# Kernel optimization log

Hardware: AMD Instinct MI355X
Metric: run time of the kernel (lower is better)

Reference implementation:

```python
import jax, jax.numpy as jnp
import numpy as np

HIDDEN = 1024
INTER = 2048
NUM_EXPERTS = 8
TOP_K = 2
GROUP_SIZE = 128
TOKENS = 4096


def _dequant_int4(packed, scale, group_size):
    # packed: [E, N, K//2] ints in [0,256) holding two uint4 nibbles (low | high<<4)
    # scale:  [E, N, K//group_size] float32
    E, N, Kh = packed.shape
    K = 2 * Kh
    low = packed & 0xF
    high = (packed >> 4) & 0xF
    # interleave: even K positions = low nibble, odd = high nibble
    q = jnp.stack([low, high], axis=-1).reshape(E, N, K) - 8  # int4 values in [-8,7]
    q = q.astype(jnp.float32).reshape(E, N, K // group_size, group_size)
    w = q * scale[..., None]
    return w.reshape(E, N, K)


def setup_inputs() -> dict:
    key = jax.random.key(0)
    k1, k2, k3, k4, k5, k6 = jax.random.split(key, 6)
    x = jax.random.normal(k1, (TOKENS, HIDDEN), dtype=jnp.float32)
    router_w = jax.random.normal(k2, (NUM_EXPERTS, HIDDEN), dtype=jnp.float32) * 0.02
    w1 = jax.random.randint(k3, (NUM_EXPERTS, 2 * INTER, HIDDEN // 2), 0, 256, dtype=jnp.int32)
    w1_scale = jax.random.uniform(k4, (NUM_EXPERTS, 2 * INTER, HIDDEN // GROUP_SIZE), dtype=jnp.float32) * 0.05
    w2 = jax.random.randint(k5, (NUM_EXPERTS, HIDDEN, INTER // 2), 0, 256, dtype=jnp.int32)
    w2_scale = jax.random.uniform(k6, (NUM_EXPERTS, HIDDEN, INTER // GROUP_SIZE), dtype=jnp.float32) * 0.05
    return {"x": x, "router_w": router_w, "w1": w1, "w1_scale": w1_scale, "w2": w2, "w2_scale": w2_scale}


def reference(x, router_w, w1, w1_scale, w2, w2_scale):
    # Router: topk then softmax over the top-k logits
    scores = x @ router_w.T                                 # [T, E]
    top_w, top_i = jax.lax.top_k(scores, TOP_K)             # [T, K]
    top_w = jax.nn.softmax(top_w, axis=-1).astype(jnp.float32)

    # Dequantize int4 grouped weights once
    w1_deq = _dequant_int4(w1, w1_scale, GROUP_SIZE)        # [E, 2I, H]
    w2_deq = _dequant_int4(w2, w2_scale, GROUP_SIZE)        # [E, H, I]

    out = jnp.zeros_like(x)
    for e in range(NUM_EXPERTS):
        # per-token routing weight for expert e (0 if not routed)
        ge = jnp.sum(top_w * (top_i == e), axis=-1)         # [T]
        h = x @ w1_deq[e].T                                  # [T, 2I]
        gate, up = h[:, :INTER], h[:, INTER:]
        a = jax.nn.silu(gate) * up                           # SwiGLU
        y = a @ w2_deq[e].T                                  # [T, H]
        out = out + ge[:, None] * y
    return out
```

## Files before the change

### kernel.cpp

```cpp
#include <hip/hip_runtime.h>
#include <hip/hip_bf16.h>

#define HIDDEN 1024
#define INTER 2048
#define NE 8
#define GS 128
#define TOKENS 4096
#define MAXROWS 9216
#define MAXTILES 72

typedef __bf16 bf16x8 __attribute__((ext_vector_type(8)));
typedef float f32x4 __attribute__((ext_vector_type(4)));

#define OFF_TOPKI 0u
#define OFF_TOPKW 32768u
#define OFF_CTRL  65536u
#define OFF_TOK   66048u
#define OFF_SLOT  102912u
#define OFF_TILE  135680u
#define OFF_XB    139776u
#define OFF_A     8530432u
#define OFF_W1D   46279168u
#define OFF_W2D   113388032u
#define OFF_Y0    OFF_W1D
#define OFF_Y1    (OFF_W1D + 18874368u)

__device__ __forceinline__ unsigned short f2bf(float f) {
  union { float f; unsigned int u; } v; v.f = f;
  unsigned int r = (v.u + 0x7FFFu + ((v.u >> 16) & 1u)) >> 16;
  return (unsigned short)r;
}
__device__ __forceinline__ float bf2f(unsigned int u) {
  union { unsigned int u; float f; } v; v.u = u << 16;
  return v.f;
}
__device__ __forceinline__ unsigned int pack2(unsigned short lo, unsigned short hi) {
  return (unsigned int)lo | ((unsigned int)hi << 16);
}

typedef const __attribute__((address_space(1))) unsigned int GAS;
typedef __attribute__((address_space(3))) unsigned int LAS;
__device__ __forceinline__ void gload16(const unsigned short* g, unsigned short* l) {
  __builtin_amdgcn_global_load_lds((GAS*)g, (LAS*)l, 16, 0, 0);
}


__global__ __launch_bounds__(256) void k_prep(const float* __restrict__ x,
    const float* __restrict__ rw, int* __restrict__ topki, float* __restrict__ topkw,
    const int* __restrict__ w1, const float* __restrict__ w1s,
    unsigned short* __restrict__ w1d,
    const int* __restrict__ w2, const float* __restrict__ w2s,
    unsigned short* __restrict__ w2d, unsigned short* __restrict__ xb) {
  int bid = blockIdx.x, tid = threadIdx.x;
  if (bid == 25600) {
    uint2 z; z.x = 0u; z.y = 0u;
    *reinterpret_cast<uint2*>(xb + (size_t)TOKENS * HIDDEN + tid * 4) = z;
    return;
  }
  if (bid >= 17408) {
    int gid = (bid - 17408) * 256 + tid;
    int i4 = gid * 4;
    int r = i4 >> 10;
    int i = i4 & 1023;
    float s = w2s[r * 16 + (i >> 6)];
    int4 p = *reinterpret_cast<const int4*>(w2 + (size_t)i4);
    int pv[4] = { p.x, p.y, p.z, p.w };
    uint4 o; unsigned int ov[4];
#pragma unroll
    for (int j = 0; j < 4; j++) {
      float lo = (float)((pv[j] & 15) - 8) * s;
      float hi = (float)(((pv[j] >> 4) & 15) - 8) * s;
      ov[j] = pack2(f2bf(lo), f2bf(hi));
    }
    o.x = ov[0]; o.y = ov[1]; o.z = ov[2]; o.w = ov[3];
    *reinterpret_cast<uint4*>(w2d + ((size_t)r << 11) + 2 * i) = o;
    return;
  }
  if (bid >= 1024) {
    int gid = (bid - 1024) * 256 + tid;
    int i4 = gid * 4;
    int r = i4 >> 9;
    int i = i4 & 511;
    float s = w1s[r * 8 + (i >> 6)];
    int4 p = *reinterpret_cast<const int4*>(w1 + (size_t)i4);
    int pv[4] = { p.x, p.y, p.z, p.w };
    uint4 o; unsigned int ov[4];
#pragma unroll
    for (int j = 0; j < 4; j++) {
      float lo = (float)((pv[j] & 15) - 8) * s;
      float hi = (float)(((pv[j] >> 4) & 15) - 8) * s;
      ov[j] = pack2(f2bf(lo), f2bf(hi));
    }
    o.x = ov[0]; o.y = ov[1]; o.z = ov[2]; o.w = ov[3];
    *reinterpret_cast<uint4*>(w1d + ((size_t)r << 10) + 2 * i) = o;
    return;
  }
  int wave = tid >> 6, lane = tid & 63;
  int t = bid * 4 + wave;
  float acc[NE];
#pragma unroll
  for (int e = 0; e < NE; e++) acc[e] = 0.f;
  const float* xr = x + (size_t)t * HIDDEN;
  unsigned short* xbr = xb + (size_t)t * HIDDEN;
  for (int i = lane; i < HIDDEN; i += 64) {
    float xv = xr[i];
    xbr[i] = f2bf(xv);
#pragma unroll
    for (int e = 0; e < NE; e++) acc[e] += xv * rw[e * HIDDEN + i];
  }
#pragma unroll
  for (int e = 0; e < NE; e++) {
    float v = acc[e];
    for (int off = 32; off > 0; off >>= 1) v += __shfl_down(v, off, 64);
    acc[e] = v;
  }
  if (lane == 0) {
    int b0 = 0; float s0 = acc[0];
#pragma unroll
    for (int e = 1; e < NE; e++) if (acc[e] > s0) { s0 = acc[e]; b0 = e; }
    int b1 = -1; float s1 = -3.0e38f;
#pragma unroll
    for (int e = 0; e < NE; e++) if (e != b0 && acc[e] > s1) { s1 = acc[e]; b1 = e; }
    float w0 = 1.f / (1.f + __expf(s1 - s0));
    topki[t * 2] = b0; topki[t * 2 + 1] = b1;
    topkw[t * 2] = w0; topkw[t * 2 + 1] = 1.f - w0;
  }
}

__global__ __launch_bounds__(256) void k_route2(const int* __restrict__ topki,
    int* __restrict__ ctrl, int* __restrict__ tok, int* __restrict__ slots,
    int* __restrict__ tilemap) {
  __shared__ int h[NE], off[NE], cnt[NE];
  int tid = threadIdx.x;
  if (tid < NE) h[tid] = 0;
  __syncthreads();
  for (int i = tid; i < TOKENS * 2; i += 256) atomicAdd(&h[topki[i]], 1);
  __syncthreads();
  if (tid == 0) {
    int run = 0, t = 0;
    for (int e = 0; e < NE; e++) {
      int c = h[e];
      ctrl[e] = c; ctrl[16 + e] = run; off[e] = run;
      int pc = (c + 127) & ~127;
      for (int mt = 0; mt < (pc >> 7); mt++) tilemap[t++] = (e << 20) | (run + mt * 128);
      run += pc;
    }
    ctrl[24] = run; ctrl[25] = t;
  }
  __syncthreads();
#pragma unroll
  for (int e = 0; e < NE; e++) {
    int c = h[e], pc = (c + 127) & ~127;
    for (int i = c + tid; i < pc; i += 256) tok[off[e] + i] = -1;
  }
  if (tid < NE) cnt[tid] = off[tid];
  __syncthreads();
  for (int i = tid; i < TOKENS * 2; i += 256) {
    int e = topki[i];
    int p = atomicAdd(&cnt[e], 1);
    tok[p] = i >> 1;
    slots[i] = p;
  }
}

__global__ __launch_bounds__(256) void k_gemm1(
    const unsigned short* __restrict__ xb, const unsigned short* __restrict__ w1d,
    const int* __restrict__ ctrl, const int* __restrict__ tilemap,
    const int* __restrict__ tok, unsigned short* __restrict__ a_out) {
  __shared__ unsigned short sA[128 * 32];
  __shared__ unsigned short sBg[64 * 32];
  __shared__ unsigned short sBu[64 * 32];
  int bid = blockIdx.x, tid = threadIdx.x;
  int nt = bid & 31, tile = bid >> 5;
  if (tile >= ctrl[25]) return;
  int tm = tilemap[tile];
  int e = tm >> 20, row0 = tm & 0xFFFFF;
  int n0 = nt * 64;
  int wave = tid >> 6, lane = tid & 63;
  int ln = lane & 15, quad = lane >> 4;
  int wr = (wave & 1) * 64, wc = (wave >> 1) * 32;

  int srow = tid >> 2, scblk = tid & 3;
  int scol = (scblk ^ ((srow >> 1) & 3)) * 8;
  int t0 = tok[row0 + srow];
  int t1 = tok[row0 + 64 + srow];
  const unsigned short* gA0 = xb + (size_t)(t0 < 0 ? TOKENS : t0) * HIDDEN + scol;
  const unsigned short* gA1 = xb + (size_t)(t1 < 0 ? TOKENS : t1) * HIDDEN + scol;
  const unsigned short* gBg = w1d + ((size_t)e * 4096 + n0 + srow) * HIDDEN + scol;
  const unsigned short* gBu = gBg + (size_t)INTER * HIDDEN;
  unsigned short* lA0 = sA + tid * 8;
  unsigned short* lA1 = sA + 64 * 32 + tid * 8;
  unsigned short* lBg = sBg + tid * 8;
  unsigned short* lBu = sBu + tid * 8;

  f32x4 aG[4][2] = {}, aU[4][2] = {};
  for (int k0 = 0; k0 < HIDDEN; k0 += 32) {
    __syncthreads();
    gload16(gA0 + k0, lA0);
    gload16(gA1 + k0, lA1);
    gload16(gBg + k0, lBg);
    gload16(gBu + k0, lBu);
    __syncthreads();
    bf16x8 af[4], bg[2], bu[2];
#pragma unroll
    for (int m = 0; m < 4; m++) {
      int ar = wr + m * 16 + ln;
      af[m] = *reinterpret_cast<const bf16x8*>(&sA[ar * 32 + (quad ^ ((ar >> 1) & 3)) * 8]);
    }
#pragma unroll
    for (int n = 0; n < 2; n++) {
      int br = wc + n * 16 + ln;
      int bo = br * 32 + (quad ^ ((br >> 1) & 3)) * 8;
      bg[n] = *reinterpret_cast<const bf16x8*>(&sBg[bo]);
      bu[n] = *reinterpret_cast<const bf16x8*>(&sBu[bo]);
    }
#pragma unroll
    for (int m = 0; m < 4; m++)
#pragma unroll
      for (int n = 0; n < 2; n++) {
        aG[m][n] = __builtin_amdgcn_mfma_f32_16x16x32_bf16(af[m], bg[n], aG[m][n], 0, 0, 0);
        aU[m][n] = __builtin_amdgcn_mfma_f32_16x16x32_bf16(af[m], bu[n], aU[m][n], 0, 0, 0);
      }
  }
#pragma unroll
  for (int m = 0; m < 4; m++)
#pragma unroll
    for (int n = 0; n < 2; n++) {
      int col = n0 + wc + n * 16 + ln;
#pragma unroll
      for (int r = 0; r < 4; r++) {
        float g = aG[m][n][r], u = aU[m][n][r];
        float act = (g / (1.f + __expf(-g))) * u;
        int row = row0 + wr + m * 16 + quad * 4 + r;
        a_out[(size_t)row * INTER + col] = f2bf(act);
      }
    }
}

__global__ __launch_bounds__(256) void k_gemm2(
    const unsigned short* __restrict__ a_in, const unsigned short* __restrict__ w2d,
    const int* __restrict__ ctrl, const int* __restrict__ tilemap,
    unsigned short* __restrict__ y) {
  __shared__ unsigned short sA[128 * 32];
  __shared__ unsigned short sB[128 * 32];
  int bid = blockIdx.x, tid = threadIdx.x;
  int kp = bid & 1, nt = (bid >> 1) & 7, tile = bid >> 4;
  if (tile >= ctrl[25]) return;
  int tm = tilemap[tile];
  int e = tm >> 20, row0 = tm & 0xFFFFF;
  int n0 = nt * 128;
  int wave = tid >> 6, lane = tid & 63;
  int ln = lane & 15, quad = lane >> 4;
  int wr = (wave & 1) * 64, wc = (wave >> 1) * 64;

  int srow = tid >> 2, scblk = tid & 3;
  int scol = (scblk ^ ((srow >> 1) & 3)) * 8;
  int kbase = kp * (INTER / 2);
  const unsigned short* gA0 = a_in + (size_t)(row0 + srow) * INTER + kbase + scol;
  const unsigned short* gA1 = gA0 + (size_t)64 * INTER;
  const unsigned short* gB0 = w2d + ((size_t)e * 1024 + n0 + srow) * INTER + kbase + scol;
  const unsigned short* gB1 = gB0 + (size_t)64 * INTER;
  unsigned short* lA0 = sA + tid * 8;
  unsigned short* lA1 = sA + 64 * 32 + tid * 8;
  unsigned short* lB0 = sB + tid * 8;
  unsigned short* lB1 = sB + 64 * 32 + tid * 8;

  f32x4 acc[4][4] = {};
  for (int k0 = 0; k0 < INTER / 2; k0 += 32) {
    __syncthreads();
    gload16(gA0 + k0, lA0);
    gload16(gA1 + k0, lA1);
    gload16(gB0 + k0, lB0);
    gload16(gB1 + k0, lB1);
    __syncthreads();
    bf16x8 af[4], bf_[4];
#pragma unroll
    for (int m = 0; m < 4; m++) {
      int ar = wr + m * 16 + ln;
      af[m] = *reinterpret_cast<const bf16x8*>(&sA[ar * 32 + (quad ^ ((ar >> 1) & 3)) * 8]);
    }
#pragma unroll
    for (int n = 0; n < 4; n++) {
      int br = wc + n * 16 + ln;
      bf_[n] = *reinterpret_cast<const bf16x8*>(&sB[br * 32 + (quad ^ ((br >> 1) & 3)) * 8]);
    }
#pragma unroll
    for (int m = 0; m < 4; m++)
#pragma unroll
      for (int n = 0; n < 4; n++)
        acc[m][n] = __builtin_amdgcn_mfma_f32_16x16x32_bf16(af[m], bf_[n], acc[m][n], 0, 0, 0);
  }
  unsigned short* yk = y + (size_t)kp * MAXROWS * HIDDEN;
#pragma unroll
  for (int m = 0; m < 4; m++)
#pragma unroll
    for (int n = 0; n < 4; n++) {
      int col = n0 + wc + n * 16 + ln;
#pragma unroll
      for (int r = 0; r < 4; r++) {
        int row = row0 + wr + m * 16 + quad * 4 + r;
        yk[(size_t)row * HIDDEN + col] = f2bf(acc[m][n][r]);
      }
    }
}

__global__ __launch_bounds__(256) void k_combine(const unsigned short* __restrict__ y,
    const int* __restrict__ slots, const float* __restrict__ topkw,
    float* __restrict__ out) {
  int t = blockIdx.x;
  int c = threadIdx.x * 4;
  int s0 = slots[t * 2], s1 = slots[t * 2 + 1];
  float g0 = topkw[t * 2], g1 = topkw[t * 2 + 1];
  const unsigned short* y1 = y + (size_t)MAXROWS * HIDDEN;
  uint2 a0 = *reinterpret_cast<const uint2*>(y  + (size_t)s0 * HIDDEN + c);
  uint2 a1 = *reinterpret_cast<const uint2*>(y1 + (size_t)s0 * HIDDEN + c);
  uint2 b0 = *reinterpret_cast<const uint2*>(y  + (size_t)s1 * HIDDEN + c);
  uint2 b1 = *reinterpret_cast<const uint2*>(y1 + (size_t)s1 * HIDDEN + c);
  float4 o;
  o.x = g0 * (bf2f(a0.x & 0xffffu) + bf2f(a1.x & 0xffffu))
      + g1 * (bf2f(b0.x & 0xffffu) + bf2f(b1.x & 0xffffu));
  o.y = g0 * (bf2f(a0.x >> 16) + bf2f(a1.x >> 16))
      + g1 * (bf2f(b0.x >> 16) + bf2f(b1.x >> 16));
  o.z = g0 * (bf2f(a0.y & 0xffffu) + bf2f(a1.y & 0xffffu))
      + g1 * (bf2f(b0.y & 0xffffu) + bf2f(b1.y & 0xffffu));
  o.w = g0 * (bf2f(a0.y >> 16) + bf2f(a1.y >> 16))
      + g1 * (bf2f(b0.y >> 16) + bf2f(b1.y >> 16));
  *reinterpret_cast<float4*>(out + (size_t)t * HIDDEN + c) = o;
}

extern "C" void kernel_launch(void* const* d_in, const int* in_sizes, int n_in,
                              void* d_out, int out_size, void* d_ws, size_t ws_size,
                              hipStream_t stream) {
  const float* x   = (const float*)d_in[0];
  const float* rw  = (const float*)d_in[1];
  const int*   w1  = (const int*)d_in[2];
  const float* w1s = (const float*)d_in[3];
  const int*   w2  = (const int*)d_in[4];
  const float* w2s = (const float*)d_in[5];
  float* out = (float*)d_out;
  char* ws = (char*)d_ws;

  int*   topki = (int*)(ws + OFF_TOPKI);
  float* topkw = (float*)(ws + OFF_TOPKW);
  int*   ctrl  = (int*)(ws + OFF_CTRL);
  int*   tok   = (int*)(ws + OFF_TOK);
  int*   slots = (int*)(ws + OFF_SLOT);
  int*   tilemap = (int*)(ws + OFF_TILE);
  unsigned short* xb  = (unsigned short*)(ws + OFF_XB);
  unsigned short* a   = (unsigned short*)(ws + OFF_A);
  unsigned short* w1d = (unsigned short*)(ws + OFF_W1D);
  unsigned short* w2d = (unsigned short*)(ws + OFF_W2D);
  unsigned short* y   = (unsigned short*)(ws + OFF_Y0);

  k_prep<<<25601, 256, 0, stream>>>(x, rw, topki, topkw, w1, w1s, w1d, w2, w2s, w2d, xb);
  k_route2<<<1, 256, 0, stream>>>(topki, ctrl, tok, slots, tilemap);
  k_gemm1<<<32 * MAXTILES, 256, 0, stream>>>(xb, w1d, ctrl, tilemap, tok, a);
  k_gemm2<<<16 * MAXTILES, 256, 0, stream>>>(a, w2d, ctrl, tilemap, y);
  k_combine<<<TOKENS, 256, 0, stream>>>(y, slots, topkw, out);
}
```

Before: 328.0 us.

## Pre-swizzle weights and activations into MFMA fragment layout, load directly to registers

The dequant step now writes W1 and W2 in a per-lane MFMA fragment order, and gemm1 writes its activation output in the same fragment order. The GEMMs can then load operands straight from global memory into registers with one coalesced 16-byte load per lane. Shared-memory staging is dropped for the weights in gemm1 and for both operands in gemm2, with a one-step register prefetch in place of it. This removes LDS traffic and barriers, but blocks no longer share operand loads through LDS, so each wave fetches its own data and global and L2 traffic goes up. gemm1's output stores also become scattered.

```diff
diff --git a/kernel.cpp b/kernel.cpp
--- a/kernel.cpp
+++ b/kernel.cpp
@@ -23,7 +23,6 @@
 #define OFF_W1D   46279168u
 #define OFF_W2D   113388032u
 #define OFF_Y0    OFF_W1D
-#define OFF_Y1    (OFF_W1D + 18874368u)
 
 __device__ __forceinline__ unsigned short f2bf(float f) {
   union { float f; unsigned int u; } v; v.f = f;
@@ -48,9 +47,9 @@
 __global__ __launch_bounds__(256) void k_prep(const float* __restrict__ x,
     const float* __restrict__ rw, int* __restrict__ topki, float* __restrict__ topkw,
     const int* __restrict__ w1, const float* __restrict__ w1s,
-    unsigned short* __restrict__ w1d,
+    unsigned short* __restrict__ w1f,
     const int* __restrict__ w2, const float* __restrict__ w2s,
-    unsigned short* __restrict__ w2d, unsigned short* __restrict__ xb) {
+    unsigned short* __restrict__ w2f, unsigned short* __restrict__ xb) {
   int bid = blockIdx.x, tid = threadIdx.x;
   if (bid == 25600) {
     uint2 z; z.x = 0u; z.y = 0u;
@@ -59,11 +58,11 @@
   }
   if (bid >= 17408) {
     int gid = (bid - 17408) * 256 + tid;
-    int i4 = gid * 4;
-    int r = i4 >> 10;
-    int i = i4 & 1023;
-    float s = w2s[r * 16 + (i >> 6)];
-    int4 p = *reinterpret_cast<const int4*>(w2 + (size_t)i4);
+    int lane = gid & 63, kt = (gid >> 6) & 63, ntP = (gid >> 12) & 63, e = gid >> 18;
+    int n = ntP * 16 + (lane & 15), q = lane >> 4;
+    size_t R = (size_t)e * 1024 + n;
+    float s = w2s[R * 16 + (kt >> 2)];
+    int4 p = *reinterpret_cast<const int4*>(w2 + R * 1024 + kt * 16 + q * 4);
     int pv[4] = { p.x, p.y, p.z, p.w };
     uint4 o; unsigned int ov[4];
 #pragma unroll
@@ -73,16 +72,16 @@
       ov[j] = pack2(f2bf(lo), f2bf(hi));
     }
     o.x = ov[0]; o.y = ov[1]; o.z = ov[2]; o.w = ov[3];
-    *reinterpret_cast<uint4*>(w2d + ((size_t)r << 11) + 2 * i) = o;
+    *reinterpret_cast<uint4*>(w2f + (size_t)gid * 8) = o;
     return;
   }
   if (bid >= 1024) {
     int gid = (bid - 1024) * 256 + tid;
-    int i4 = gid * 4;
-    int r = i4 >> 9;
-    int i = i4 & 511;
-    float s = w1s[r * 8 + (i >> 6)];
-    int4 p = *reinterpret_cast<const int4*>(w1 + (size_t)i4);
+    int lane = gid & 63, kt = (gid >> 6) & 31, ntP = (gid >> 11) & 255, e = gid >> 19;
+    int n = ntP * 16 + (lane & 15), q = lane >> 4;
+    size_t R = (size_t)e * 4096 + n;
+    float s = w1s[R * 8 + (kt >> 2)];
+    int4 p = *reinterpret_cast<const int4*>(w1 + R * 512 + kt * 16 + q * 4);
     int pv[4] = { p.x, p.y, p.z, p.w };
     uint4 o; unsigned int ov[4];
 #pragma unroll
@@ -92,7 +91,7 @@
       ov[j] = pack2(f2bf(lo), f2bf(hi));
     }
     o.x = ov[0]; o.y = ov[1]; o.z = ov[2]; o.w = ov[3];
-    *reinterpret_cast<uint4*>(w1d + ((size_t)r << 10) + 2 * i) = o;
+    *reinterpret_cast<uint4*>(w1f + (size_t)gid * 8) = o;
     return;
   }
   int wave = tid >> 6, lane = tid & 63;
@@ -164,18 +163,15 @@
 }
 
 __global__ __launch_bounds__(256) void k_gemm1(
-    const unsigned short* __restrict__ xb, const unsigned short* __restrict__ w1d,
+    const unsigned short* __restrict__ xb, const unsigned short* __restrict__ w1f,
     const int* __restrict__ ctrl, const int* __restrict__ tilemap,
-    const int* __restrict__ tok, unsigned short* __restrict__ a_out) {
+    const int* __restrict__ tok, unsigned short* __restrict__ a_f) {
   __shared__ unsigned short sA[128 * 32];
-  __shared__ unsigned short sBg[64 * 32];
-  __shared__ unsigned short sBu[64 * 32];
   int bid = blockIdx.x, tid = threadIdx.x;
   int nt = bid & 31, tile = bid >> 5;
   if (tile >= ctrl[25]) return;
   int tm = tilemap[tile];
   int e = tm >> 20, row0 = tm & 0xFFFFF;
-  int n0 = nt * 64;
   int wave = tid >> 6, lane = tid & 63;
   int ln = lane & 15, quad = lane >> 4;
   int wr = (wave & 1) * 64, wc = (wave >> 1) * 32;
@@ -186,63 +182,69 @@
   int t1 = tok[row0 + 64 + srow];
   const unsigned short* gA0 = xb + (size_t)(t0 < 0 ? TOKENS : t0) * HIDDEN + scol;
   const unsigned short* gA1 = xb + (size_t)(t1 < 0 ? TOKENS : t1) * HIDDEN + scol;
-  const unsigned short* gBg = w1d + ((size_t)e * 4096 + n0 + srow) * HIDDEN + scol;
-  const unsigned short* gBu = gBg + (size_t)INTER * HIDDEN;
   unsigned short* lA0 = sA + tid * 8;
   unsigned short* lA1 = sA + 64 * 32 + tid * 8;
-  unsigned short* lBg = sBg + tid * 8;
-  unsigned short* lBu = sBu + tid * 8;
+
+  int ntPg = nt * 4 + (wave >> 1) * 2;
+  const unsigned short* pbg0 = w1f + (size_t)(e * 256 + ntPg) * 16384 + lane * 8;
+  const unsigned short* pbg1 = w1f + (size_t)(e * 256 + ntPg + 1) * 16384 + lane * 8;
+  const unsigned short* pbu0 = w1f + (size_t)(e * 256 + 128 + ntPg) * 16384 + lane * 8;
+  const unsigned short* pbu1 = w1f + (size_t)(e * 256 + 128 + ntPg + 1) * 16384 + lane * 8;
+
+  bf16x8 bgc[2], buc[2];
+  bgc[0] = *reinterpret_cast<const bf16x8*>(pbg0);
+  bgc[1] = *reinterpret_cast<const bf16x8*>(pbg1);
+  buc[0] = *reinterpret_cast<const bf16x8*>(pbu0);
+  buc[1] = *reinterpret_cast<const bf16x8*>(pbu1);
 
   f32x4 aG[4][2] = {}, aU[4][2] = {};
-  for (int k0 = 0; k0 < HIDDEN; k0 += 32) {
+#pragma unroll 2
+  for (int kt = 0; kt < 32; kt++) {
     __syncthreads();
-    gload16(gA0 + k0, lA0);
-    gload16(gA1 + k0, lA1);
-    gload16(gBg + k0, lBg);
-    gload16(gBu + k0, lBu);
+    gload16(gA0 + kt * 32, lA0);
+    gload16(gA1 + kt * 32, lA1);
     __syncthreads();
-    bf16x8 af[4], bg[2], bu[2];
+    int o = (kt < 31) ? (kt + 1) * 512 : 0;
+    bf16x8 bgn0 = *reinterpret_cast<const bf16x8*>(pbg0 + o);
+    bf16x8 bgn1 = *reinterpret_cast<const bf16x8*>(pbg1 + o);
+    bf16x8 bun0 = *reinterpret_cast<const bf16x8*>(pbu0 + o);
+    bf16x8 bun1 = *reinterpret_cast<const bf16x8*>(pbu1 + o);
+    bf16x8 af[4];
 #pragma unroll
     for (int m = 0; m < 4; m++) {
       int ar = wr + m * 16 + ln;
       af[m] = *reinterpret_cast<const bf16x8*>(&sA[ar * 32 + (quad ^ ((ar >> 1) & 3)) * 8]);
     }
 #pragma unroll
+    for (int m = 0; m < 4; m++) {
+      aG[m][0] = __builtin_amdgcn_mfma_f32_16x16x32_bf16(af[m], bgc[0], aG[m][0], 0, 0, 0);
+      aG[m][1] = __builtin_amdgcn_mfma_f32_16x16x32_bf16(af[m], bgc[1], aG[m][1], 0, 0, 0);
+      aU[m][0] = __builtin_amdgcn_mfma_f32_16x16x32_bf16(af[m], buc[0], aU[m][0], 0, 0, 0);
+      aU[m][1] = __builtin_amdgcn_mfma_f32_16x16x32_bf16(af[m], buc[1], aU[m][1], 0, 0, 0);
+    }
+    bgc[0] = bgn0; bgc[1] = bgn1; buc[0] = bun0; buc[1] = bun1;
+  }
+#pragma unroll
+  for (int m = 0; m < 4; m++)
+#pragma unroll
     for (int n = 0; n < 2; n++) {
-      int br = wc + n * 16 + ln;
-      int bo = br * 32 + (quad ^ ((br >> 1) & 3)) * 8;
-      bg[n] = *reinterpret_cast<const bf16x8*>(&sBg[bo]);
-      bu[n] = *reinterpret_cast<const bf16x8*>(&sBu[bo]);
-    }
-#pragma unroll
-    for (int m = 0; m < 4; m++)
-#pragma unroll
-      for (int n = 0; n < 2; n++) {
-        aG[m][n] = __builtin_amdgcn_mfma_f32_16x16x32_bf16(af[m], bg[n], aG[m][n], 0, 0, 0);
-        aU[m][n] = __builtin_amdgcn_mfma_f32_16x16x32_bf16(af[m], bu[n], aU[m][n], 0, 0, 0);
-      }
-  }
-#pragma unroll
-  for (int m = 0; m < 4; m++)
-#pragma unroll
-    for (int n = 0; n < 2; n++) {
-      int col = n0 + wc + n * 16 + ln;
+      int c = nt * 64 + wc + n * 16 + ln;
+      int kta = c >> 5, qa = (c >> 3) & 3, ja = c & 7;
 #pragma unroll
       for (int r = 0; r < 4; r++) {
         float g = aG[m][n][r], u = aU[m][n][r];
         float act = (g / (1.f + __expf(-g))) * u;
         int row = row0 + wr + m * 16 + quad * 4 + r;
-        a_out[(size_t)row * INTER + col] = f2bf(act);
+        size_t idx = ((size_t)((row >> 4) * 64 + kta) * 64 + qa * 16 + (row & 15)) * 8 + ja;
+        a_f[idx] = f2bf(act);
       }
     }
 }
 
 __global__ __launch_bounds__(256) void k_gemm2(
-    const unsigned short* __restrict__ a_in, const unsigned short* __restrict__ w2d,
+    const unsigned short* __restrict__ a_f, const unsigned short* __restrict__ w2f,
     const int* __restrict__ ctrl, const int* __restrict__ tilemap,
     unsigned short* __restrict__ y) {
-  __shared__ unsigned short sA[128 * 32];
-  __shared__ unsigned short sB[128 * 32];
   int bid = blockIdx.x, tid = threadIdx.x;
   int kp = bid & 1, nt = (bid >> 1) & 7, tile = bid >> 4;
   if (tile >= ctrl[25]) return;
@@ -253,42 +255,41 @@
   int ln = lane & 15, quad = lane >> 4;
   int wr = (wave & 1) * 64, wc = (wave >> 1) * 64;
 
-  int srow = tid >> 2, scblk = tid & 3;
-  int scol = (scblk ^ ((srow >> 1) & 3)) * 8;
-  int kbase = kp * (INTER / 2);
-  const unsigned short* gA0 = a_in + (size_t)(row0 + srow) * INTER + kbase + scol;
-  const unsigned short* gA1 = gA0 + (size_t)64 * INTER;
-  const unsigned short* gB0 = w2d + ((size_t)e * 1024 + n0 + srow) * INTER + kbase + scol;
-  const unsigned short* gB1 = gB0 + (size_t)64 * INTER;
-  unsigned short* lA0 = sA + tid * 8;
-  unsigned short* lA1 = sA + 64 * 32 + tid * 8;
-  unsigned short* lB0 = sB + tid * 8;
-  unsigned short* lB1 = sB + 64 * 32 + tid * 8;
+  int rt0 = (row0 >> 4) + (wave & 1) * 4;
+  int ntP0 = nt * 8 + (wave >> 1) * 4;
+  const unsigned short* pa[4];
+  const unsigned short* pb[4];
+#pragma unroll
+  for (int m = 0; m < 4; m++)
+    pa[m] = a_f + ((size_t)(rt0 + m) * 64 + kp * 32) * 512 + lane * 8;
+#pragma unroll
+  for (int n = 0; n < 4; n++)
+    pb[n] = w2f + ((size_t)(e * 64 + ntP0 + n) * 64 + kp * 32) * 512 + lane * 8;
+
+  bf16x8 ac[4], bc[4];
+#pragma unroll
+  for (int m = 0; m < 4; m++) ac[m] = *reinterpret_cast<const bf16x8*>(pa[m]);
+#pragma unroll
+  for (int n = 0; n < 4; n++) bc[n] = *reinterpret_cast<const bf16x8*>(pb[n]);
 
   f32x4 acc[4][4] = {};
-  for (int k0 = 0; k0 < INTER / 2; k0 += 32) {
-    __syncthreads();
-    gload16(gA0 + k0, lA0);
-    gload16(gA1 + k0, lA1);
-    gload16(gB0 + k0, lB0);
-    gload16(gB1 + k0, lB1);
-    __syncthreads();
-    bf16x8 af[4], bf_[4];
-#pragma unroll
-    for (int m = 0; m < 4; m++) {
-      int ar = wr + m * 16 + ln;
-      af[m] = *reinterpret_cast<const bf16x8*>(&sA[ar * 32 + (quad ^ ((ar >> 1) & 3)) * 8]);
-    }
-#pragma unroll
-    for (int n = 0; n < 4; n++) {
-      int br = wc + n * 16 + ln;
-      bf_[n] = *reinterpret_cast<const bf16x8*>(&sB[br * 32 + (quad ^ ((br >> 1) & 3)) * 8]);
-    }
+#pragma unroll 2
+  for (int i = 0; i < 32; i++) {
+    int o = (i < 31) ? (i + 1) * 512 : 0;
+    bf16x8 an[4], bn[4];
+#pragma unroll
+    for (int m = 0; m < 4; m++) an[m] = *reinterpret_cast<const bf16x8*>(pa[m] + o);
+#pragma unroll
+    for (int n = 0; n < 4; n++) bn[n] = *reinterpret_cast<const bf16x8*>(pb[n] + o);
 #pragma unroll
     for (int m = 0; m < 4; m++)
 #pragma unroll
       for (int n = 0; n < 4; n++)
-        acc[m][n] = __builtin_amdgcn_mfma_f32_16x16x32_bf16(af[m], bf_[n], acc[m][n], 0, 0, 0);
+        acc[m][n] = __builtin_amdgcn_mfma_f32_16x16x32_bf16(ac[m], bc[n], acc[m][n], 0, 0, 0);
+#pragma unroll
+    for (int m = 0; m < 4; m++) ac[m] = an[m];
+#pragma unroll
+    for (int n = 0; n < 4; n++) bc[n] = bn[n];
   }
   unsigned short* yk = y + (size_t)kp * MAXROWS * HIDDEN;
 #pragma unroll
@@ -347,14 +348,14 @@
   int*   slots = (int*)(ws + OFF_SLOT);
   int*   tilemap = (int*)(ws + OFF_TILE);
   unsigned short* xb  = (unsigned short*)(ws + OFF_XB);
-  unsigned short* a   = (unsigned short*)(ws + OFF_A);
-  unsigned short* w1d = (unsigned short*)(ws + OFF_W1D);
-  unsigned short* w2d = (unsigned short*)(ws + OFF_W2D);
+  unsigned short* a_f = (unsigned short*)(ws + OFF_A);
+  unsigned short* w1f = (unsigned short*)(ws + OFF_W1D);
+  unsigned short* w2f = (unsigned short*)(ws + OFF_W2D);
   unsigned short* y   = (unsigned short*)(ws + OFF_Y0);
 
-  k_prep<<<25601, 256, 0, stream>>>(x, rw, topki, topkw, w1, w1s, w1d, w2, w2s, w2d, xb);
+  k_prep<<<25601, 256, 0, stream>>>(x, rw, topki, topkw, w1, w1s, w1f, w2, w2s, w2f, xb);
   k_route2<<<1, 256, 0, stream>>>(topki, ctrl, tok, slots, tilemap);
-  k_gemm1<<<32 * MAXTILES, 256, 0, stream>>>(xb, w1d, ctrl, tilemap, tok, a);
-  k_gemm2<<<16 * MAXTILES, 256, 0, stream>>>(a, w2d, ctrl, tilemap, y);
+  k_gemm1<<<32 * MAXTILES, 256, 0, stream>>>(xb, w1f, ctrl, tilemap, tok, a_f);
+  k_gemm2<<<16 * MAXTILES, 256, 0, stream>>>(a_f, w2f, ctrl, tilemap, y);
   k_combine<<<TOKENS, 256, 0, stream>>>(y, slots, topkw, out);
 }
```

Measured after the change: 351.5 us. 1.07x slower.
